# Optimization experiments

Hardware: AMD Instinct MI355X
Metric: run time of the kernel (lower is better)

Reference implementation:

```python
import jax, jax.numpy as jnp
import numpy as np

EPS = 1e-6
EPS_SQR = EPS ** 2
RADIO = 0.7  # init kwarg
W_STAGE0 = 0.5


def _ohem_mean(diff_flat, k):
    """diff_flat: [B, N] nonneg values; k: [B] int32 per-sample top-k count.
    Equivalent to: mean_i( sum(topk(diff_flat[i], k[i])) / (k[i] + EPS) ).
    Implemented jit-compatibly via descending sort + cumsum + gather."""
    N = diff_flat.shape[-1]
    sorted_desc = -jnp.sort(-diff_flat, axis=-1)          # [B, N]
    csum = jnp.cumsum(sorted_desc, axis=-1)               # [B, N]
    idx = jnp.clip(k - 1, 0, N - 1)
    sum_k = jnp.take_along_axis(csum, idx[:, None], axis=-1)[:, 0]
    sum_k = jnp.where(k > 0, sum_k, jnp.zeros_like(sum_k))
    loss = sum_k / (k.astype(diff_flat.dtype) + EPS)
    return jnp.mean(loss)


def setup_inputs() -> dict:
    key = jax.random.key(0)
    ks = jax.random.split(key, 6)
    B, H, W = 8, 512, 512
    image = jax.random.uniform(ks[0], (B, 3, H, W), dtype=jnp.float32)
    alpha = jax.random.uniform(ks[1], (B, 1, H, W), dtype=jnp.float32) * 255.0  # 0..255 like GT alpha
    raw_alpha_pred = jax.random.uniform(ks[2], (B, 1, H, W), dtype=jnp.float32)
    fg = jax.random.uniform(ks[3], (B, 3, H, W), dtype=jnp.float32)
    bg = jax.random.uniform(ks[4], (B, 3, H, W), dtype=jnp.float32)
    trimap = jax.random.randint(ks[5], (B, 1, H, W), 0, 2, dtype=jnp.int32) * 128  # {0,128}
    return {"image": image, "alpha": alpha, "raw_alpha_pred": raw_alpha_pred,
            "trimap": trimap, "fg": fg, "bg": bg}


def reference(image, alpha, raw_alpha_pred, trimap, fg, bg):
    B = trimap.shape[0]
    unknown = (trimap == 128).astype(image.dtype)          # [B,1,H,W]
    count = jnp.sum(unknown.reshape(B, -1), axis=-1)       # per-sample unknown pixel count
    k = jnp.floor(count * RADIO).astype(jnp.int32)         # torch: int(pred_num * radio)

    # ---- alpha prediction loss ----
    d = (alpha / 255.0 - raw_alpha_pred) * unknown         # [B,1,H,W]
    d = jnp.sqrt(d * d + EPS_SQR)
    alpha_loss = _ohem_mean(d.reshape(B, -1), k)

    # ---- compositional loss ----
    pred_img = fg * raw_alpha_pred + (1.0 - raw_alpha_pred) * bg   # [B,3,H,W]
    dc = (image - pred_img) * unknown                      # mask broadcasts over 3 channels
    dc = jnp.sqrt(dc * dc + EPS_SQR)
    dc = dc.sum(axis=1)                                    # [B,H,W]
    comp_loss = _ohem_mean(dc.reshape(B, -1), k)

    return W_STAGE0 * alpha_loss + (1.0 - W_STAGE0) * comp_loss
```

## Files before the change

### kernel.cpp

```cpp
#include <hip/hip_runtime.h>
#include <math.h>

#define NB 8
#define NPIX 262144
#define NBINS 2048
#define NBINS2 256
#define TPB 256
#define TPB2 512
#define BPS 64
#define PPB (NPIX / BPS)
#define BPU2 16
#define CPB2 (NPIX / BPU2)
#define EPS2 1e-12f

struct SelState { unsigned b1; unsigned rem; unsigned k; unsigned pad; };

#define F4E(v,j) (((const float*)&(v))[j])
#define I4E(v,j) (((const int*)&(v))[j])

__device__ __forceinline__ void pixel_vals(float a, float p,
                                           float i0, float i1, float i2,
                                           float f0, float f1, float f2,
                                           float g0, float g1, float g2,
                                           float& d, float& dc)
{
    float diff = a * (1.0f / 255.0f) - p;
    d = sqrtf(diff * diff + EPS2);
    float om = 1.0f - p;
    float e0 = i0 - (f0 * p + om * g0);
    float e1 = i1 - (f1 * p + om * g1);
    float e2 = i2 - (f2 * p + om * g2);
    dc = sqrtf(e0 * e0 + EPS2) + sqrtf(e1 * e1 + EPS2) + sqrtf(e2 * e2 + EPS2);
}

__global__ __launch_bounds__(TPB) void k_pass1(
    const float* __restrict__ image, const float* __restrict__ alpha,
    const float* __restrict__ pred, const int* __restrict__ trimap,
    const float* __restrict__ fg, const float* __restrict__ bg,
    unsigned* __restrict__ gcnt, unsigned* __restrict__ h1c, float* __restrict__ vals)
{
    __shared__ unsigned hc[2 * NBINS];
    const int tid = threadIdx.x;
    for (int i = tid; i < 2 * NBINS; i += TPB) hc[i] = 0u;
    __syncthreads();

    const int s = blockIdx.x / BPS;
    const int chunk = blockIdx.x % BPS;
    const int pbase = s * NPIX + chunk * PPB;
    const int cbase = s * 3 * NPIX + chunk * PPB;
    float* vd = vals + (s * 2 + 0) * NPIX + chunk * PPB;
    float* vc = vals + (s * 2 + 1) * NPIX + chunk * PPB;

    const float md  = sqrtf(EPS2);
    const float mdc = md + md + md;

    unsigned nUnk = 0, nMask = 0;

    for (int it = 0; it < PPB / (TPB * 4); ++it) {
        const int off = (it * TPB + tid) * 4;
        int4   tm = *(const int4*)(trimap + pbase + off);
        float4 al = *(const float4*)(alpha + pbase + off);
        float4 pr = *(const float4*)(pred + pbase + off);
        float4 i0 = *(const float4*)(image + cbase + off);
        float4 i1 = *(const float4*)(image + cbase + NPIX + off);
        float4 i2 = *(const float4*)(image + cbase + 2 * NPIX + off);
        float4 f0 = *(const float4*)(fg + cbase + off);
        float4 f1 = *(const float4*)(fg + cbase + NPIX + off);
        float4 f2 = *(const float4*)(fg + cbase + 2 * NPIX + off);
        float4 g0 = *(const float4*)(bg + cbase + off);
        float4 g1 = *(const float4*)(bg + cbase + NPIX + off);
        float4 g2 = *(const float4*)(bg + cbase + 2 * NPIX + off);
        float4 od, oc;
#pragma unroll
        for (int j = 0; j < 4; ++j) {
            float d, dc;
            if (I4E(tm, j) == 128) {
                ++nUnk;
                pixel_vals(F4E(al, j), F4E(pr, j),
                           F4E(i0, j), F4E(i1, j), F4E(i2, j),
                           F4E(f0, j), F4E(f1, j), F4E(f2, j),
                           F4E(g0, j), F4E(g1, j), F4E(g2, j), d, dc);
                atomicAdd(&hc[__float_as_uint(d) >> 21], 1u);
                atomicAdd(&hc[NBINS + (__float_as_uint(dc) >> 21)], 1u);
            } else {
                ++nMask;
                d = md; dc = mdc;
            }
            ((float*)&od)[j] = d;
            ((float*)&oc)[j] = dc;
        }
        *(float4*)(vd + off) = od;
        *(float4*)(vc + off) = oc;
    }

    unsigned u = nUnk, m = nMask;
#pragma unroll
    for (int o = 32; o > 0; o >>= 1) { u += __shfl_down(u, o); m += __shfl_down(m, o); }
    __shared__ unsigned wred[8];
    const int wave = tid >> 6;
    if ((tid & 63) == 0) { wred[wave * 2] = u; wred[wave * 2 + 1] = m; }
    __syncthreads();
    if (tid == 0) {
        unsigned U = 0, M = 0;
        for (int w = 0; w < 4; ++w) { U += wred[w * 2]; M += wred[w * 2 + 1]; }
        atomicAdd(&gcnt[s], U);
        if (M) {
            atomicAdd(&hc[__float_as_uint(md) >> 21], M);
            atomicAdd(&hc[NBINS + (__float_as_uint(mdc) >> 21)], M);
        }
    }
    __syncthreads();

    for (int i = tid; i < 2 * NBINS; i += TPB) {
        unsigned c = hc[i];
        if (c) {
            int arr = (i >= NBINS) ? 1 : 0;
            int b = i & (NBINS - 1);
            atomicAdd(&h1c[(s * 2 + arr) * NBINS + b], c);
        }
    }
}

__global__ __launch_bounds__(TPB) void k_select1(
    const unsigned* __restrict__ gcnt, const unsigned* __restrict__ h1c,
    SelState* __restrict__ st)
{
    const int unit = blockIdx.x;
    const int s = unit >> 1;
    const int t = threadIdx.x;
    const unsigned* hc = h1c + unit * NBINS;
    unsigned count = gcnt[s];
    int k = (int)floorf((float)count * 0.7f);

    __shared__ unsigned spc[TPB];
    unsigned pc = 0;
#pragma unroll
    for (int j = 0; j < NBINS / TPB; ++j) pc += hc[t * (NBINS / TPB) + j];
    spc[t] = pc;
    __syncthreads();
    __shared__ unsigned sufc[TPB + 1];
    if (t == 0) {
        unsigned c = 0;
        sufc[TPB] = 0;
        for (int i = TPB - 1; i >= 0; --i) { c += spc[i]; sufc[i] = c; }
    }
    __syncthreads();
    if (k <= 0) {
        if (t == 0) { st[unit].b1 = 0xFFFFFFFFu; st[unit].rem = 0; st[unit].k = 0; }
        return;
    }
    unsigned above = sufc[t + 1];
    if (above < (unsigned)k && (unsigned)k <= sufc[t]) {
        unsigned c = above;
        int b1 = t * (NBINS / TPB);
        for (int j = NBINS / TPB - 1; j >= 0; --j) {
            unsigned bcn = hc[t * (NBINS / TPB) + j];
            if (c + bcn >= (unsigned)k) { b1 = t * (NBINS / TPB) + j; break; }
            c += bcn;
        }
        st[unit].b1 = (unsigned)b1;
        st[unit].rem = (unsigned)k - c;
        st[unit].k = (unsigned)k;
    }
}

__global__ __launch_bounds__(TPB2) void k_pass2(
    const float* __restrict__ vals, const SelState* __restrict__ st,
    float* __restrict__ hpriv, float* __restrict__ sumgt)
{
    const int unit = blockIdx.x >> 4;
    const int chunk = blockIdx.x & (BPU2 - 1);
    const SelState S = st[unit];
    if (S.b1 == 0xFFFFFFFFu) return;

    __shared__ unsigned hcnt[NBINS2];
    __shared__ float    hsum[NBINS2];
    const int tid = threadIdx.x;
    if (tid < NBINS2) { hcnt[tid] = 0u; hsum[tid] = 0.f; }
    __syncthreads();

    const float* v = vals + unit * NPIX + chunk * CPB2;
    float lsum = 0.f;
#pragma unroll
    for (int it = 0; it < CPB2 / (TPB2 * 4); ++it) {
        const int off = (it * TPB2 + tid) * 4;
        float4 x = *(const float4*)(v + off);
#pragma unroll
        for (int j = 0; j < 4; ++j) {
            float val = F4E(x, j);
            unsigned bits = __float_as_uint(val);
            unsigned b = bits >> 21;
            if (b > S.b1) {
                lsum += val;
            } else if (b == S.b1) {
                unsigned sb = (bits >> 13) & (NBINS2 - 1);
                atomicAdd(&hcnt[sb], 1u);
                atomicAdd(&hsum[sb], val);
            }
        }
    }
#pragma unroll
    for (int o = 32; o > 0; o >>= 1) lsum += __shfl_down(lsum, o);
    __shared__ float wred[TPB2 / 64];
    const int wave = tid >> 6;
    if ((tid & 63) == 0) wred[wave] = lsum;
    __syncthreads();
    if (tid == 0) {
        float tot = 0.f;
        for (int w = 0; w < TPB2 / 64; ++w) tot += wred[w];
        atomicAdd(&sumgt[unit], tot);
    }
    float* outp = hpriv + (size_t)(unit * BPU2 + chunk) * (2 * NBINS2);
    if (tid < NBINS2) {
        outp[tid] = (float)hcnt[tid];
        outp[NBINS2 + tid] = hsum[tid];
    }
}

__global__ __launch_bounds__(TPB) void k_select2_final(
    const float* __restrict__ hpriv, const SelState* __restrict__ st,
    const float* __restrict__ sumgt, float* __restrict__ out)
{
    const int unit = blockIdx.x;
    const int t = threadIdx.x;
    const SelState S = st[unit];
    if (S.b1 == 0xFFFFFFFFu) return;

    __shared__ unsigned cnt[NBINS2];
    __shared__ float    sm[NBINS2];
    float c = 0.f, s = 0.f;
    const float* base = hpriv + (size_t)unit * BPU2 * (2 * NBINS2);
    for (int ch = 0; ch < BPU2; ++ch) {
        c += base[ch * (2 * NBINS2) + t];
        s += base[ch * (2 * NBINS2) + NBINS2 + t];
    }
    cnt[t] = (unsigned)c;
    sm[t]  = s;
    __syncthreads();
    __shared__ unsigned sufc[NBINS2 + 1];
    __shared__ float    sufs[NBINS2 + 1];
    if (t == 0) {
        unsigned cc = 0; float ss = 0.f;
        sufc[NBINS2] = 0; sufs[NBINS2] = 0.f;
        for (int i = NBINS2 - 1; i >= 0; --i) { cc += cnt[i]; ss += sm[i]; sufc[i] = cc; sufs[i] = ss; }
    }
    __syncthreads();
    unsigned k = S.rem;
    unsigned above = sufc[t + 1];
    if (above < k && k <= sufc[t]) {
        unsigned rem2 = k - above;
        float avg = sm[t] / (float)cnt[t];
        float sum_k = sumgt[unit] + sufs[t + 1] + (float)rem2 * avg;
        float loss = sum_k / ((float)S.k + 1e-6f);
        atomicAdd(out, 0.0625f * loss);
    }
}

extern "C" void kernel_launch(void* const* d_in, const int* in_sizes, int n_in,
                              void* d_out, int out_size, void* d_ws, size_t ws_size,
                              hipStream_t stream)
{
    const float* image  = (const float*)d_in[0];
    const float* alpha  = (const float*)d_in[1];
    const float* pred   = (const float*)d_in[2];
    const int*   trimap = (const int*)d_in[3];
    const float* fg     = (const float*)d_in[4];
    const float* bg     = (const float*)d_in[5];
    float* out = (float*)d_out;

    char* ws = (char*)d_ws;
    unsigned* gcnt = (unsigned*)(ws);
    unsigned* h1c  = (unsigned*)(ws + 64);
    float*    sumgt= (float*)(ws + 64 + 131072);
    SelState* st   = (SelState*)(ws + 64 + 131072 + 64);
    float*    vals = (float*)(ws + 262144);
    float*    hpriv= (float*)(ws + 262144 + (size_t)NB * 2 * NPIX * 4);
    const size_t zbytes = 64 + 131072 + 64;

    hipMemsetAsync(d_ws, 0, zbytes, stream);
    hipMemsetAsync(d_out, 0, sizeof(float), stream);
    k_pass1<<<NB * BPS, TPB, 0, stream>>>(image, alpha, pred, trimap, fg, bg, gcnt, h1c, vals);
    k_select1<<<NB * 2, TPB, 0, stream>>>(gcnt, h1c, st);
    k_pass2<<<NB * 2 * BPU2, TPB2, 0, stream>>>(vals, st, hpriv, sumgt);
    k_select2_final<<<NB * 2, TPB, 0, stream>>>(hpriv, st, sumgt, out);
}
```

Baseline: 157.0 us.

## Fuse selection passes into one persistent kernel with grid barriers and register-held values

```diff
diff --git a/kernel.cpp b/kernel.cpp
--- a/kernel.cpp
+++ b/kernel.cpp
@@ -3,20 +3,20 @@
 
 #define NB 8
 #define NPIX 262144
-#define NBINS 2048
+#define BPSAMP 64
+#define NBLK (NB * BPSAMP)
+#define TPB 256
+#define PPT 16
+#define PPB (TPB * PPT)
+#define NBINS 1024
+#define BPT (NBINS / TPB)
 #define NBINS2 256
-#define TPB 256
-#define TPB2 512
-#define BPS 64
-#define PPB (NPIX / BPS)
-#define BPU2 16
-#define CPB2 (NPIX / BPU2)
 #define EPS2 1e-12f
-
-struct SelState { unsigned b1; unsigned rem; unsigned k; unsigned pad; };
 
 #define F4E(v,j) (((const float*)&(v))[j])
 #define I4E(v,j) (((const int*)&(v))[j])
+
+struct Sel { unsigned b1, rem, k; };
 
 __device__ __forceinline__ void pixel_vals(float a, float p,
                                            float i0, float i1, float i2,
@@ -33,30 +33,94 @@
     dc = sqrtf(e0 * e0 + EPS2) + sqrtf(e1 * e1 + EPS2) + sqrtf(e2 * e2 + EPS2);
 }
 
-__global__ __launch_bounds__(TPB) void k_pass1(
+__device__ void gridbar(unsigned* __restrict__ bar, int slot)
+{
+    __syncthreads();
+    if (threadIdx.x == 0) {
+        __threadfence();
+        unsigned arrived = atomicAdd(&bar[slot * 2], 1u);
+        if (arrived == (unsigned)(NBLK - 1)) {
+            atomicAdd(&bar[slot * 2 + 1], 1u);
+        } else {
+            while (atomicAdd(&bar[slot * 2 + 1], 0u) == 0u)
+                __builtin_amdgcn_s_sleep(8);
+        }
+        __threadfence();
+    }
+    __syncthreads();
+}
+
+__device__ void select_unit(const unsigned* __restrict__ hc, unsigned k,
+                            unsigned* sufB, unsigned* bcast, Sel& out)
+{
+    const int t = threadIdx.x;
+    unsigned bins[BPT];
+    unsigned pc = 0;
+#pragma unroll
+    for (int j = 0; j < BPT; ++j) { bins[j] = hc[t * BPT + j]; pc += bins[j]; }
+    sufB[t] = pc;
+    __syncthreads();
+    for (int off = 1; off < TPB; off <<= 1) {
+        unsigned add = (t + off < TPB) ? sufB[t + off] : 0u;
+        __syncthreads();
+        sufB[t] += add;
+        __syncthreads();
+    }
+    unsigned suf = sufB[t];
+    if (t == 0) { bcast[0] = 0xFFFFFFFFu; bcast[1] = 0u; bcast[2] = 0u; }
+    __syncthreads();
+    if (k > 0) {
+        unsigned above = suf - pc;
+        if (above < k && k <= suf) {
+            unsigned c = above; int b1 = -1;
+#pragma unroll
+            for (int j = BPT - 1; j >= 0; --j) {
+                if (b1 < 0) {
+                    if (c + bins[j] >= k) b1 = t * BPT + j;
+                    else c += bins[j];
+                }
+            }
+            bcast[0] = (unsigned)b1; bcast[1] = k - c; bcast[2] = k;
+        }
+    }
+    __syncthreads();
+    out.b1 = bcast[0]; out.rem = bcast[1]; out.k = bcast[2];
+    __syncthreads();
+}
+
+__global__ __launch_bounds__(TPB, 4) void k_fused(
     const float* __restrict__ image, const float* __restrict__ alpha,
     const float* __restrict__ pred, const int* __restrict__ trimap,
     const float* __restrict__ fg, const float* __restrict__ bg,
-    unsigned* __restrict__ gcnt, unsigned* __restrict__ h1c, float* __restrict__ vals)
+    unsigned* __restrict__ bar, unsigned* __restrict__ gcnt,
+    unsigned* __restrict__ h1c, float* __restrict__ hpriv,
+    float* __restrict__ sgl, float* __restrict__ out)
 {
     __shared__ unsigned hc[2 * NBINS];
+    __shared__ unsigned scnt[2 * NBINS2];
+    __shared__ float    ssum[2 * NBINS2];
+    __shared__ unsigned sufB[TPB];
+    __shared__ float    sufF[TPB];
+    __shared__ unsigned bcast[4];
+    __shared__ float    fred[8];
+
     const int tid = threadIdx.x;
+    const int b = blockIdx.x;
+    const int s = b / BPSAMP;
+    const int ch = b % BPSAMP;
+
     for (int i = tid; i < 2 * NBINS; i += TPB) hc[i] = 0u;
-    __syncthreads();
-
-    const int s = blockIdx.x / BPS;
-    const int chunk = blockIdx.x % BPS;
-    const int pbase = s * NPIX + chunk * PPB;
-    const int cbase = s * 3 * NPIX + chunk * PPB;
-    float* vd = vals + (s * 2 + 0) * NPIX + chunk * PPB;
-    float* vc = vals + (s * 2 + 1) * NPIX + chunk * PPB;
-
-    const float md  = sqrtf(EPS2);
-    const float mdc = md + md + md;
-
-    unsigned nUnk = 0, nMask = 0;
-
-    for (int it = 0; it < PPB / (TPB * 4); ++it) {
+    for (int i = tid; i < 2 * NBINS2; i += TPB) { scnt[i] = 0u; ssum[i] = 0.f; }
+    __syncthreads();
+
+    const int pbase = s * NPIX + ch * PPB;
+    const int cbase = s * 3 * NPIX + ch * PPB;
+    float dv[PPT], cv[PPT];
+    unsigned unkm = 0;
+    unsigned nUnk = 0;
+
+#pragma unroll
+    for (int it = 0; it < PPT / 4; ++it) {
         const int off = (it * TPB + tid) * 4;
         int4   tm = *(const int4*)(trimap + pbase + off);
         float4 al = *(const float4*)(alpha + pbase + off);
@@ -70,189 +134,130 @@
         float4 g0 = *(const float4*)(bg + cbase + off);
         float4 g1 = *(const float4*)(bg + cbase + NPIX + off);
         float4 g2 = *(const float4*)(bg + cbase + 2 * NPIX + off);
-        float4 od, oc;
 #pragma unroll
         for (int j = 0; j < 4; ++j) {
-            float d, dc;
+            const int vi = it * 4 + j;
+            float d = 0.f, c = 0.f;
             if (I4E(tm, j) == 128) {
                 ++nUnk;
+                unkm |= 1u << vi;
                 pixel_vals(F4E(al, j), F4E(pr, j),
                            F4E(i0, j), F4E(i1, j), F4E(i2, j),
                            F4E(f0, j), F4E(f1, j), F4E(f2, j),
-                           F4E(g0, j), F4E(g1, j), F4E(g2, j), d, dc);
+                           F4E(g0, j), F4E(g1, j), F4E(g2, j), d, c);
                 atomicAdd(&hc[__float_as_uint(d) >> 21], 1u);
-                atomicAdd(&hc[NBINS + (__float_as_uint(dc) >> 21)], 1u);
-            } else {
-                ++nMask;
-                d = md; dc = mdc;
-            }
-            ((float*)&od)[j] = d;
-            ((float*)&oc)[j] = dc;
-        }
-        *(float4*)(vd + off) = od;
-        *(float4*)(vc + off) = oc;
-    }
-
-    unsigned u = nUnk, m = nMask;
-#pragma unroll
-    for (int o = 32; o > 0; o >>= 1) { u += __shfl_down(u, o); m += __shfl_down(m, o); }
-    __shared__ unsigned wred[8];
-    const int wave = tid >> 6;
-    if ((tid & 63) == 0) { wred[wave * 2] = u; wred[wave * 2 + 1] = m; }
+                atomicAdd(&hc[NBINS + (__float_as_uint(c) >> 21)], 1u);
+            }
+            dv[vi] = d; cv[vi] = c;
+        }
+    }
+
+    unsigned u = nUnk;
+#pragma unroll
+    for (int o = 32; o > 0; o >>= 1) u += __shfl_down(u, o);
+    if ((tid & 63) == 0) sufB[tid >> 6] = u;
+    __syncthreads();
+    if (tid == 0) atomicAdd(&gcnt[s], sufB[0] + sufB[1] + sufB[2] + sufB[3]);
+    __syncthreads();
+
+    for (int i = tid; i < 2 * NBINS; i += TPB) {
+        unsigned cc = hc[i];
+        if (cc) atomicAdd(&h1c[(s * 2 + (i >= NBINS ? 1 : 0)) * NBINS + (i & (NBINS - 1))], cc);
+    }
+
+    gridbar(bar, 0);
+
+    unsigned K = gcnt[s];
+    unsigned kk = (unsigned)(int)floorf((float)K * 0.7f);
+    Sel Sd, Sc;
+    select_unit(h1c + (s * 2 + 0) * NBINS, kk, sufB, bcast, Sd);
+    select_unit(h1c + (s * 2 + 1) * NBINS, kk, sufB, bcast, Sc);
+
+    float lsd = 0.f, lsc = 0.f;
+#pragma unroll
+    for (int vi = 0; vi < PPT; ++vi) {
+        if (unkm & (1u << vi)) {
+            unsigned bits = __float_as_uint(dv[vi]);
+            unsigned bd = bits >> 21;
+            if (Sd.b1 != 0xFFFFFFFFu) {
+                if (bd > Sd.b1) lsd += dv[vi];
+                else if (bd == Sd.b1) {
+                    unsigned sb = (bits >> 13) & (NBINS2 - 1);
+                    atomicAdd(&scnt[sb], 1u);
+                    atomicAdd(&ssum[sb], dv[vi]);
+                }
+            }
+            unsigned cbits = __float_as_uint(cv[vi]);
+            unsigned bc = cbits >> 21;
+            if (Sc.b1 != 0xFFFFFFFFu) {
+                if (bc > Sc.b1) lsc += cv[vi];
+                else if (bc == Sc.b1) {
+                    unsigned sb = (cbits >> 13) & (NBINS2 - 1);
+                    atomicAdd(&scnt[NBINS2 + sb], 1u);
+                    atomicAdd(&ssum[NBINS2 + sb], cv[vi]);
+                }
+            }
+        }
+    }
+#pragma unroll
+    for (int o = 32; o > 0; o >>= 1) { lsd += __shfl_down(lsd, o); lsc += __shfl_down(lsc, o); }
+    if ((tid & 63) == 0) { fred[tid >> 6] = lsd; fred[4 + (tid >> 6)] = lsc; }
     __syncthreads();
     if (tid == 0) {
-        unsigned U = 0, M = 0;
-        for (int w = 0; w < 4; ++w) { U += wred[w * 2]; M += wred[w * 2 + 1]; }
-        atomicAdd(&gcnt[s], U);
-        if (M) {
-            atomicAdd(&hc[__float_as_uint(md) >> 21], M);
-            atomicAdd(&hc[NBINS + (__float_as_uint(mdc) >> 21)], M);
-        }
-    }
-    __syncthreads();
-
-    for (int i = tid; i < 2 * NBINS; i += TPB) {
-        unsigned c = hc[i];
-        if (c) {
-            int arr = (i >= NBINS) ? 1 : 0;
-            int b = i & (NBINS - 1);
-            atomicAdd(&h1c[(s * 2 + arr) * NBINS + b], c);
-        }
-    }
-}
-
-__global__ __launch_bounds__(TPB) void k_select1(
-    const unsigned* __restrict__ gcnt, const unsigned* __restrict__ h1c,
-    SelState* __restrict__ st)
-{
-    const int unit = blockIdx.x;
-    const int s = unit >> 1;
-    const int t = threadIdx.x;
-    const unsigned* hc = h1c + unit * NBINS;
-    unsigned count = gcnt[s];
-    int k = (int)floorf((float)count * 0.7f);
-
-    __shared__ unsigned spc[TPB];
-    unsigned pc = 0;
-#pragma unroll
-    for (int j = 0; j < NBINS / TPB; ++j) pc += hc[t * (NBINS / TPB) + j];
-    spc[t] = pc;
-    __syncthreads();
-    __shared__ unsigned sufc[TPB + 1];
-    if (t == 0) {
-        unsigned c = 0;
-        sufc[TPB] = 0;
-        for (int i = TPB - 1; i >= 0; --i) { c += spc[i]; sufc[i] = c; }
-    }
-    __syncthreads();
-    if (k <= 0) {
-        if (t == 0) { st[unit].b1 = 0xFFFFFFFFu; st[unit].rem = 0; st[unit].k = 0; }
-        return;
-    }
-    unsigned above = sufc[t + 1];
-    if (above < (unsigned)k && (unsigned)k <= sufc[t]) {
-        unsigned c = above;
-        int b1 = t * (NBINS / TPB);
-        for (int j = NBINS / TPB - 1; j >= 0; --j) {
-            unsigned bcn = hc[t * (NBINS / TPB) + j];
-            if (c + bcn >= (unsigned)k) { b1 = t * (NBINS / TPB) + j; break; }
-            c += bcn;
-        }
-        st[unit].b1 = (unsigned)b1;
-        st[unit].rem = (unsigned)k - c;
-        st[unit].k = (unsigned)k;
-    }
-}
-
-__global__ __launch_bounds__(TPB2) void k_pass2(
-    const float* __restrict__ vals, const SelState* __restrict__ st,
-    float* __restrict__ hpriv, float* __restrict__ sumgt)
-{
-    const int unit = blockIdx.x >> 4;
-    const int chunk = blockIdx.x & (BPU2 - 1);
-    const SelState S = st[unit];
-    if (S.b1 == 0xFFFFFFFFu) return;
-
-    __shared__ unsigned hcnt[NBINS2];
-    __shared__ float    hsum[NBINS2];
-    const int tid = threadIdx.x;
-    if (tid < NBINS2) { hcnt[tid] = 0u; hsum[tid] = 0.f; }
-    __syncthreads();
-
-    const float* v = vals + unit * NPIX + chunk * CPB2;
-    float lsum = 0.f;
-#pragma unroll
-    for (int it = 0; it < CPB2 / (TPB2 * 4); ++it) {
-        const int off = (it * TPB2 + tid) * 4;
-        float4 x = *(const float4*)(v + off);
-#pragma unroll
-        for (int j = 0; j < 4; ++j) {
-            float val = F4E(x, j);
-            unsigned bits = __float_as_uint(val);
-            unsigned b = bits >> 21;
-            if (b > S.b1) {
-                lsum += val;
-            } else if (b == S.b1) {
-                unsigned sb = (bits >> 13) & (NBINS2 - 1);
-                atomicAdd(&hcnt[sb], 1u);
-                atomicAdd(&hsum[sb], val);
-            }
-        }
-    }
-#pragma unroll
-    for (int o = 32; o > 0; o >>= 1) lsum += __shfl_down(lsum, o);
-    __shared__ float wred[TPB2 / 64];
-    const int wave = tid >> 6;
-    if ((tid & 63) == 0) wred[wave] = lsum;
-    __syncthreads();
-    if (tid == 0) {
-        float tot = 0.f;
-        for (int w = 0; w < TPB2 / 64; ++w) tot += wred[w];
-        atomicAdd(&sumgt[unit], tot);
-    }
-    float* outp = hpriv + (size_t)(unit * BPU2 + chunk) * (2 * NBINS2);
-    if (tid < NBINS2) {
-        outp[tid] = (float)hcnt[tid];
-        outp[NBINS2 + tid] = hsum[tid];
-    }
-}
-
-__global__ __launch_bounds__(TPB) void k_select2_final(
-    const float* __restrict__ hpriv, const SelState* __restrict__ st,
-    const float* __restrict__ sumgt, float* __restrict__ out)
-{
-    const int unit = blockIdx.x;
-    const int t = threadIdx.x;
-    const SelState S = st[unit];
-    if (S.b1 == 0xFFFFFFFFu) return;
-
-    __shared__ unsigned cnt[NBINS2];
-    __shared__ float    sm[NBINS2];
-    float c = 0.f, s = 0.f;
-    const float* base = hpriv + (size_t)unit * BPU2 * (2 * NBINS2);
-    for (int ch = 0; ch < BPU2; ++ch) {
-        c += base[ch * (2 * NBINS2) + t];
-        s += base[ch * (2 * NBINS2) + NBINS2 + t];
-    }
-    cnt[t] = (unsigned)c;
-    sm[t]  = s;
-    __syncthreads();
-    __shared__ unsigned sufc[NBINS2 + 1];
-    __shared__ float    sufs[NBINS2 + 1];
-    if (t == 0) {
-        unsigned cc = 0; float ss = 0.f;
-        sufc[NBINS2] = 0; sufs[NBINS2] = 0.f;
-        for (int i = NBINS2 - 1; i >= 0; --i) { cc += cnt[i]; ss += sm[i]; sufc[i] = cc; sufs[i] = ss; }
-    }
-    __syncthreads();
-    unsigned k = S.rem;
-    unsigned above = sufc[t + 1];
-    if (above < k && k <= sufc[t]) {
-        unsigned rem2 = k - above;
-        float avg = sm[t] / (float)cnt[t];
-        float sum_k = sumgt[unit] + sufs[t + 1] + (float)rem2 * avg;
-        float loss = sum_k / ((float)S.k + 1e-6f);
-        atomicAdd(out, 0.0625f * loss);
+        sgl[(size_t)(s * BPSAMP + ch) * 2 + 0] = fred[0] + fred[1] + fred[2] + fred[3];
+        sgl[(size_t)(s * BPSAMP + ch) * 2 + 1] = fred[4] + fred[5] + fred[6] + fred[7];
+    }
+    {
+        float* hp = hpriv + (size_t)(s * BPSAMP + ch) * (4 * NBINS2);
+        hp[0 * NBINS2 + tid] = (float)scnt[tid];
+        hp[1 * NBINS2 + tid] = ssum[tid];
+        hp[2 * NBINS2 + tid] = (float)scnt[NBINS2 + tid];
+        hp[3 * NBINS2 + tid] = ssum[NBINS2 + tid];
+    }
+
+    gridbar(bar, 1);
+
+    if (b < 2 * NB) {
+        const int uu = b, ss = uu >> 1, arr = uu & 1;
+        unsigned K2 = gcnt[ss];
+        unsigned kk2 = (unsigned)(int)floorf((float)K2 * 0.7f);
+        Sel S;
+        select_unit(h1c + uu * NBINS, kk2, sufB, bcast, S);
+        if (S.b1 != 0xFFFFFFFFu) {
+            float cc = 0.f, sm = 0.f;
+            for (int c2 = 0; c2 < BPSAMP; ++c2) {
+                const float* hp = hpriv + (size_t)(ss * BPSAMP + c2) * (4 * NBINS2) + arr * 2 * NBINS2;
+                cc += hp[tid];
+                sm += hp[NBINS2 + tid];
+            }
+            sufF[tid] = (tid < BPSAMP) ? sgl[(size_t)(ss * BPSAMP + tid) * 2 + arr] : 0.f;
+            __syncthreads();
+            for (int off = TPB / 2; off > 0; off >>= 1) {
+                if (tid < off) sufF[tid] += sufF[tid + off];
+                __syncthreads();
+            }
+            float Ltot = sufF[0];
+            __syncthreads();
+            unsigned myc = (unsigned)cc;
+            sufB[tid] = myc; sufF[tid] = sm;
+            __syncthreads();
+            for (int off = 1; off < TPB; off <<= 1) {
+                unsigned ac = (tid + off < TPB) ? sufB[tid + off] : 0u;
+                float    as = (tid + off < TPB) ? sufF[tid + off] : 0.f;
+                __syncthreads();
+                sufB[tid] += ac; sufF[tid] += as;
+                __syncthreads();
+            }
+            unsigned suf = sufB[tid];
+            unsigned above = suf - myc;
+            if (above < S.rem && S.rem <= suf) {
+                unsigned rem2 = S.rem - above;
+                float avg = sm / (float)myc;
+                float sum_k = Ltot + (sufF[tid] - sm) + (float)rem2 * avg;
+                float loss = sum_k / ((float)S.k + 1e-6f);
+                atomicAdd(out, 0.0625f * loss);
+            }
+        }
     }
 }
 
@@ -269,18 +274,15 @@
     float* out = (float*)d_out;
 
     char* ws = (char*)d_ws;
-    unsigned* gcnt = (unsigned*)(ws);
-    unsigned* h1c  = (unsigned*)(ws + 64);
-    float*    sumgt= (float*)(ws + 64 + 131072);
-    SelState* st   = (SelState*)(ws + 64 + 131072 + 64);
-    float*    vals = (float*)(ws + 262144);
-    float*    hpriv= (float*)(ws + 262144 + (size_t)NB * 2 * NPIX * 4);
-    const size_t zbytes = 64 + 131072 + 64;
+    unsigned* bar   = (unsigned*)(ws);
+    unsigned* gcnt  = (unsigned*)(ws + 64);
+    unsigned* h1c   = (unsigned*)(ws + 128);
+    float*    sgl   = (float*)(ws + 128 + 65536);
+    float*    hpriv = (float*)(ws + 131072);
+    const size_t zbytes = 128 + 65536;
 
     hipMemsetAsync(d_ws, 0, zbytes, stream);
     hipMemsetAsync(d_out, 0, sizeof(float), stream);
-    k_pass1<<<NB * BPS, TPB, 0, stream>>>(image, alpha, pred, trimap, fg, bg, gcnt, h1c, vals);
-    k_select1<<<NB * 2, TPB, 0, stream>>>(gcnt, h1c, st);
-    k_pass2<<<NB * 2 * BPU2, TPB2, 0, stream>>>(vals, st, hpriv, sumgt);
-    k_select2_final<<<NB * 2, TPB, 0, stream>>>(hpriv, st, sumgt, out);
-}
+    k_fused<<<NBLK, TPB, 0, stream>>>(image, alpha, pred, trimap, fg, bg,
+                                      bar, gcnt, h1c, hpriv, sgl, out);
+}
```

Result: slower. 234.3 us (+49.3%).
